# Kernel optimization log

Measured on AMD Instinct MI355X. Metric: run time of the kernel, lower is better.

The kernel has to match this reference:

```python
import jax, jax.numpy as jnp
import numpy as np

B, N, DIM = 1, 1024, 512
H, DH = 8, 64
TOPK_RATIO = 0.1
SCALE = DH ** -0.5
PH = 32  # phase MLP hidden = hidden_dim//2 = 64//2
INIT_SCALE = 0.02


def cayley(Mre, Mim):
    # CayleyLinear: unitary weight W = (I - A)^{-1} (I + A), A skew-Hermitian
    M = (Mre + 1j * Mim).astype(jnp.complex64) * INIT_SCALE
    A = M - M.conj().T
    I = jnp.eye(M.shape[0], dtype=M.dtype)
    return jnp.linalg.solve(I - A, I + A)


def phase_fn(mag, pw1, pb1, pw2, pb2):
    # PhaseModulation: MLP(|alpha|) + 0.1*|alpha| residual
    h = jax.nn.silu(mag[..., None] @ pw1 + pb1)  # (...,PH)
    out = (h @ pw2 + pb2)[..., 0]
    return out + mag * 0.1


def setup_inputs() -> dict:
    key = jax.random.key(0)
    ks = jax.random.split(key, 12)
    d = {
        'x_real': jax.random.normal(ks[0], (B, N, DIM), dtype=jnp.float32),
        'x_imag': jax.random.normal(ks[1], (B, N, DIM), dtype=jnp.float32),
    }
    for i, n in enumerate(['Wq', 'Wk', 'Wv', 'Wo']):
        d[n + '_re'] = jax.random.normal(ks[2 + 2 * i], (DIM, DIM), dtype=jnp.float32)
        d[n + '_im'] = jax.random.normal(ks[3 + 2 * i], (DIM, DIM), dtype=jnp.float32)
    d['pw1'] = jax.random.normal(ks[10], (1, PH), dtype=jnp.float32) * 0.1
    d['pb1'] = jnp.zeros((PH,), dtype=jnp.float32)
    d['pw2'] = jax.random.normal(ks[11], (PH, 1), dtype=jnp.float32) * 0.1
    d['pb2'] = jnp.zeros((1,), dtype=jnp.float32)
    return d


def reference(x_real, x_imag, Wq_re, Wq_im, Wk_re, Wk_im, Wv_re, Wv_im,
              Wo_re, Wo_im, pw1, pb1, pw2, pb2):
    x = (x_real + 1j * x_imag).astype(jnp.complex64)  # (B,N,D)
    Q = x @ cayley(Wq_re, Wq_im)
    K = x @ cayley(Wk_re, Wk_im)
    V = x @ cayley(Wv_re, Wv_im)
    # (B,N,D) -> (B,H,N,DH)
    Q = Q.reshape(B, N, H, DH).transpose(0, 2, 1, 3)
    K = K.reshape(B, N, H, DH).transpose(0, 2, 1, 3)
    V = V.reshape(B, N, H, DH).transpose(0, 2, 1, 3)
    # complex inner products: conj(Q) . K
    alpha = jnp.einsum('bhnd,bhsd->bhns', Q.conj(), K) * SCALE  # (B,H,N,N) complex
    mag = jnp.abs(alpha)
    phase = phase_fn(jax.lax.stop_gradient(mag), pw1, pb1, pw2, pb2)
    beta = alpha * jnp.exp(1j * phase.astype(jnp.complex64))
    # Born-rule normalization: p = |beta|^2 / sum |beta|^2
    b2 = beta.real ** 2 + beta.imag ** 2
    probs = b2 / b2.sum(axis=-1, keepdims=True)  # (B,H,N,N) real
    # top-k interference routing
    k = max(1, int(TOPK_RATIO * N))
    tp, ti = jax.lax.top_k(probs, k)  # (B,H,N,k)
    tpn = tp / (tp.sum(axis=-1, keepdims=True) + 1e-8)
    w = jax.nn.softmax(tpn * k, axis=-1)  # complex_softmax on real input
    # gather V rows per (b,h): (N,DH)[(N,k)] -> (N,k,DH), no NxN expand
    gather = jax.vmap(jax.vmap(lambda v, i: v[i]))
    V_topk = gather(V, ti)  # (B,H,N,k,DH) complex
    out = (w[..., None] * V_topk).sum(axis=3)  # (B,H,N,DH)
    out = out.transpose(0, 2, 1, 3).reshape(B, N, DIM)
    out = out @ cayley(Wo_re, Wo_im)
    return out  # complex64 (B,N,DIM)
```

## Files before the change

### kernel.cpp

```cpp
#include <hip/hip_runtime.h>
#include <math.h>


#define PLANE   262144
#define CMAT    524288
#define PPLANE  524288
#define CPROJ   1048576
#define KTOP    102

#define R_FLOATS 12582912
#define POOL_FLOATS (4*CMAT + 8192 + R_FLOATS)
__device__ __attribute__((aligned(256))) float g_pool[POOL_FLOATS];

__launch_bounds__(256)
__global__ void cgemm_kernel(
    const float* __restrict__ Are, const float* __restrict__ Aim, int sA,
    const float* __restrict__ Bre, const float* __restrict__ Bim, int sB,
    const float* __restrict__ Dre, const float* __restrict__ Dim, int sD,
    const float* __restrict__ Ere2, float* __restrict__ Ewr, int sE,
    float* __restrict__ Cre, float* __restrict__ Cim, int sC,
    int M, int N, int Kd, float dcoef, int mode, int out_floats)
{
    __shared__ float As_re[32][34], As_im[32][34];
    __shared__ float Bs_re[32][68], Bs_im[32][68];
    const int b = blockIdx.z;
    Are += (size_t)b * sA; Aim += (size_t)b * sA;
    Bre += (size_t)b * sB; Bim += (size_t)b * sB;
    Dre += (size_t)b * sD; Dim += (size_t)b * sD;
    const float* Ere = Ere2 + (size_t)b * sE;
    const float* Eim = Ere + PLANE;
    float* Uwr = Ewr ? (Ewr + (size_t)b * sE) : (float*)0;
    Cre += (size_t)b * sC; Cim += (size_t)b * sC;
    const int tid = threadIdx.x;
    const int bm = blockIdx.y * 32, bn = blockIdx.x * 64;
    const int tm = (tid >> 4) << 1;
    const int tn = (tid & 15) << 2;
    const int lmA = tid >> 3;
    const int lkA = (tid & 7) << 2;
    const int lkB = tid >> 4;
    const int lnB = (tid & 15) << 2;
    float cr[2][4] = {{0.f}}, ci[2][4] = {{0.f}};
    const float* pAre = Are + (size_t)(bm + lmA) * Kd + lkA;
    const float* pAim = Aim + (size_t)(bm + lmA) * Kd + lkA;
    const float* pBre = Bre + (size_t)lkB * N + bn + lnB;
    const float* pBim = Bim + (size_t)lkB * N + bn + lnB;
    for (int k0 = 0; k0 < Kd; k0 += 32) {
        const float4 ar = *(const float4*)(pAre + k0);
        const float4 ai = *(const float4*)(pAim + k0);
        const float4 br0 = *(const float4*)(pBre + (size_t)k0 * N);
        const float4 bi0 = *(const float4*)(pBim + (size_t)k0 * N);
        const float4 br1 = *(const float4*)(pBre + (size_t)(k0 + 16) * N);
        const float4 bi1 = *(const float4*)(pBim + (size_t)(k0 + 16) * N);
        __syncthreads();
        As_re[lkA+0][lmA] = ar.x; As_re[lkA+1][lmA] = ar.y;
        As_re[lkA+2][lmA] = ar.z; As_re[lkA+3][lmA] = ar.w;
        As_im[lkA+0][lmA] = ai.x; As_im[lkA+1][lmA] = ai.y;
        As_im[lkA+2][lmA] = ai.z; As_im[lkA+3][lmA] = ai.w;
        *(float4*)&Bs_re[lkB][lnB] = br0;
        *(float4*)&Bs_im[lkB][lnB] = bi0;
        *(float4*)&Bs_re[lkB+16][lnB] = br1;
        *(float4*)&Bs_im[lkB+16][lnB] = bi1;
        __syncthreads();
        #pragma unroll
        for (int k = 0; k < 32; ++k) {
            const float2 xr = *(const float2*)&As_re[k][tm];
            const float2 xi = *(const float2*)&As_im[k][tm];
            const float4 yr = *(const float4*)&Bs_re[k][tn];
            const float4 yi = *(const float4*)&Bs_im[k][tn];
            const float axr[2] = {xr.x, xr.y};
            const float axi[2] = {xi.x, xi.y};
            const float byr[4] = {yr.x, yr.y, yr.z, yr.w};
            const float byi[4] = {yi.x, yi.y, yi.z, yi.w};
            #pragma unroll
            for (int i = 0; i < 2; ++i) {
                #pragma unroll
                for (int j = 0; j < 4; ++j) {
                    cr[i][j] += axr[i]*byr[j] - axi[i]*byi[j];
                    ci[i][j] += axr[i]*byi[j] + axi[i]*byr[j];
                }
            }
        }
    }
    #pragma unroll
    for (int i = 0; i < 2; ++i) {
        const int row = bm + tm + i;
        const size_t idx = (size_t)row * N + bn + tn;
        float vr[4] = {cr[i][0], cr[i][1], cr[i][2], cr[i][3]};
        float vi[4] = {ci[i][0], ci[i][1], ci[i][2], ci[i][3]};
        if (mode == 1) {
            const float4 dr4 = *(const float4*)(Dre + idx);
            const float4 di4 = *(const float4*)(Dim + idx);
            const float dr[4] = {dr4.x, dr4.y, dr4.z, dr4.w};
            const float di[4] = {di4.x, di4.y, di4.z, di4.w};
            #pragma unroll
            for (int j = 0; j < 4; ++j) { vr[j] = dcoef*dr[j] - vr[j]; vi[j] = dcoef*di[j] - vi[j]; }
        } else if (mode == 2) {
            const float4 dr4 = *(const float4*)(Dre + idx);
            const float4 di4 = *(const float4*)(Dim + idx);
            const float dr[4] = {dr4.x, dr4.y, dr4.z, dr4.w};
            const float di[4] = {di4.x, di4.y, di4.z, di4.w};
            float ur[4], ui[4];
            #pragma unroll
            for (int j = 0; j < 4; ++j) { ur[j] = 5.5f*dr[j] + 0.5f*vr[j]; ui[j] = 5.5f*di[j] + 0.5f*vi[j]; }
            *(float4*)(Uwr + idx) = make_float4(ur[0], ur[1], ur[2], ur[3]);
            *(float4*)(Uwr + PLANE + idx) = make_float4(ui[0], ui[1], ui[2], ui[3]);
        } else if (mode == 3) {
            const float inv61 = 1.0f/61.5f;
            const float4 sr4 = *(const float4*)(Dre + idx);
            const float4 si4 = *(const float4*)(Dim + idx);
            const float4 s2r = *(const float4*)(Ere + idx);
            const float4 s2i = *(const float4*)(Eim + idx);
            const float sr[4] = {sr4.x, sr4.y, sr4.z, sr4.w};
            const float si[4] = {si4.x, si4.y, si4.z, si4.w};
            const float tr[4] = {s2r.x, s2r.y, s2r.z, s2r.w};
            const float ti[4] = {s2i.x, s2i.y, s2i.z, s2i.w};
            #pragma unroll
            for (int j = 0; j < 4; ++j) {
                const float diag = (row == bn + tn + j) ? 60.5f : 0.0f;
                vr[j] = (diag + 48.f*sr[j] + 23.f*tr[j] + vr[j]) * inv61;
                vi[j] = (       48.f*si[j] + 23.f*ti[j] + vi[j]) * inv61;
            }
        } else if (mode == 4) {
            const float4 dr4 = *(const float4*)(Dre + idx);
            const float4 di4 = *(const float4*)(Dim + idx);
            const float dr[4] = {dr4.x, dr4.y, dr4.z, dr4.w};
            const float di[4] = {di4.x, di4.y, di4.z, di4.w};
            #pragma unroll
            for (int j = 0; j < 4; ++j) {
                const float diag = (row == bn + tn + j) ? 1.0f : 0.0f;
                vr[j] = 2.f*dr[j] + 2.f*vr[j] - diag;
                vi[j] = 2.f*di[j] + 2.f*vi[j];
            }
        }
        if (mode == 5) {
            #pragma unroll
            for (int j = 0; j < 4; ++j) {
                const size_t ire = idx + j;
                const size_t iim = (size_t)PPLANE + idx + j;
                if (ire < (size_t)out_floats) Cre[ire] = vr[j];
                if (iim < (size_t)out_floats) Cre[iim] = vi[j];
            }
        } else {
            *(float4*)(Cre + idx) = make_float4(vr[0], vr[1], vr[2], vr[3]);
            *(float4*)(Cim + idx) = make_float4(vi[0], vi[1], vi[2], vi[3]);
        }
    }
}

__launch_bounds__(256)
__global__ void build_A_kernel(const float* __restrict__ W0re, const float* __restrict__ W0im,
                               const float* __restrict__ W1re, const float* __restrict__ W1im,
                               const float* __restrict__ W2re, const float* __restrict__ W2im,
                               const float* __restrict__ W3re, const float* __restrict__ W3im,
                               int aoff)
{
    float* Aout = g_pool + aoff;
    const int w = blockIdx.y;
    const float* Mre; const float* Mim;
    if      (w == 0) { Mre = W0re; Mim = W0im; }
    else if (w == 1) { Mre = W1re; Mim = W1im; }
    else if (w == 2) { Mre = W2re; Mim = W2im; }
    else             { Mre = W3re; Mim = W3im; }
    const int idx = blockIdx.x * 256 + threadIdx.x;
    const int i = idx >> 9, j = idx & 511;
    float* Are = Aout + (size_t)w * CMAT;
    float* Aim = Are + PLANE;
    Are[idx] = 0.02f * (Mre[i*512 + j] - Mre[j*512 + i]);
    Aim[idx] = 0.02f * (Mim[i*512 + j] + Mim[j*512 + i]);
}

__launch_bounds__(256)
__global__ void zero_kernel(float* __restrict__ p, int n)
{
    const int i = blockIdx.x * 256 + threadIdx.x;
    if (i < n) p[i] = 0.f;
}

__launch_bounds__(256)
__global__ void scores_kernel(const float* __restrict__ Qre, const float* __restrict__ Qim,
                              const float* __restrict__ Kre, const float* __restrict__ Kim,
                              float* __restrict__ B2, float* __restrict__ RS)
{
    __shared__ float Qs_re[16][68], Qs_im[16][68], Ks_re[16][68], Ks_im[16][68];
    __shared__ float rs[64];
    const int h = blockIdx.z;
    const int bm = blockIdx.y * 64, bn = blockIdx.x * 64;
    const int tid = threadIdx.x;
    const int tm = (tid >> 4) << 2, tn = (tid & 15) << 2;
    const int lm = tid >> 2, lk = (tid & 3) << 2;
    float dr[4][4] = {{0.f}}, di[4][4] = {{0.f}};
    for (int k0 = 0; k0 < 64; k0 += 16) {
        const float4 qr = *(const float4*)(Qre + (size_t)(bm+lm)*512 + h*64 + k0 + lk);
        const float4 qi = *(const float4*)(Qim + (size_t)(bm+lm)*512 + h*64 + k0 + lk);
        const float4 kr = *(const float4*)(Kre + (size_t)(bn+lm)*512 + h*64 + k0 + lk);
        const float4 ki = *(const float4*)(Kim + (size_t)(bn+lm)*512 + h*64 + k0 + lk);
        __syncthreads();
        Qs_re[lk+0][lm]=qr.x; Qs_re[lk+1][lm]=qr.y; Qs_re[lk+2][lm]=qr.z; Qs_re[lk+3][lm]=qr.w;
        Qs_im[lk+0][lm]=qi.x; Qs_im[lk+1][lm]=qi.y; Qs_im[lk+2][lm]=qi.z; Qs_im[lk+3][lm]=qi.w;
        Ks_re[lk+0][lm]=kr.x; Ks_re[lk+1][lm]=kr.y; Ks_re[lk+2][lm]=kr.z; Ks_re[lk+3][lm]=kr.w;
        Ks_im[lk+0][lm]=ki.x; Ks_im[lk+1][lm]=ki.y; Ks_im[lk+2][lm]=ki.z; Ks_im[lk+3][lm]=ki.w;
        __syncthreads();
        #pragma unroll
        for (int k = 0; k < 16; ++k) {
            const float4 xr = *(const float4*)&Qs_re[k][tm];
            const float4 xi = *(const float4*)&Qs_im[k][tm];
            const float4 yr = *(const float4*)&Ks_re[k][tn];
            const float4 yi = *(const float4*)&Ks_im[k][tn];
            const float axr[4] = {xr.x, xr.y, xr.z, xr.w};
            const float axi[4] = {xi.x, xi.y, xi.z, xi.w};
            const float byr[4] = {yr.x, yr.y, yr.z, yr.w};
            const float byi[4] = {yi.x, yi.y, yi.z, yi.w};
            #pragma unroll
            for (int i = 0; i < 4; ++i) {
                #pragma unroll
                for (int j = 0; j < 4; ++j) {
                    dr[i][j] += axr[i]*byr[j] + axi[i]*byi[j];
                    di[i][j] += axr[i]*byi[j] - axi[i]*byr[j];
                }
            }
        }
    }
    if (tid < 64) rs[tid] = 0.f;
    __syncthreads();
    float rpart[4] = {0.f, 0.f, 0.f, 0.f};
    #pragma unroll
    for (int i = 0; i < 4; ++i) {
        #pragma unroll
        for (int j = 0; j < 4; ++j) {
            const float b2v = (dr[i][j]*dr[i][j] + di[i][j]*di[i][j]) * 0.015625f;
            B2[(size_t)h*1048576 + (size_t)(bm+tm+i)*1024 + (bn+tn+j)] = b2v;
            rpart[i] += b2v;
        }
    }
    #pragma unroll
    for (int i = 0; i < 4; ++i) atomicAdd(&rs[tm+i], rpart[i]);
    __syncthreads();
    if (tid < 64) atomicAdd(&RS[h*1024 + bm + tid], rs[tid]);
}

__launch_bounds__(256)
__global__ void select_kernel(const float* __restrict__ B2, const float* __restrict__ RS,
                              const float* __restrict__ Vre, const float* __restrict__ Vim,
                              float* __restrict__ AOre, float* __restrict__ AOim)
{
    __shared__ float sv[1024];
    __shared__ unsigned int hist[256];
    __shared__ int ssum[256];
    __shared__ unsigned int sc[4];
    __shared__ float sel_v[104];
    __shared__ int sel_i[104];
    __shared__ float sel_w[104];
    __shared__ float rbuf[256];
    const int bid = blockIdx.x;
    const int h = bid >> 10, n = bid & 1023;
    const int tid = threadIdx.x;
    const float* row = B2 + (size_t)h * 1048576 + (size_t)n * 1024;
    #pragma unroll
    for (int e = 0; e < 4; ++e) sv[tid + 256*e] = row[tid + 256*e];
    if (tid == 0) sc[2] = 0u;
    __syncthreads();

    unsigned prefix = 0u, pmask = 0u;
    int krem = KTOP;
    for (int pass = 0; pass < 4; ++pass) {
        const int shift = 24 - 8 * pass;
        hist[tid] = 0u;
        __syncthreads();
        #pragma unroll
        for (int e = 0; e < 4; ++e) {
            const unsigned u = __float_as_uint(sv[tid + 256*e]);
            if ((u & pmask) == prefix) atomicAdd(&hist[(u >> shift) & 255u], 1u);
        }
        __syncthreads();
        ssum[tid] = (int)hist[tid];
        __syncthreads();
        for (int off = 1; off < 256; off <<= 1) {
            const int add = (tid + off < 256) ? ssum[tid + off] : 0;
            __syncthreads();
            ssum[tid] += add;
            __syncthreads();
        }
        const int above = (tid < 255) ? ssum[tid + 1] : 0;
        if (ssum[tid] >= krem && above < krem) {
            sc[0] = (unsigned)tid;
            sc[1] = (unsigned)(krem - above);
        }
        __syncthreads();
        prefix |= sc[0] << shift;
        pmask |= 0xFFu << shift;
        krem = (int)sc[1];
        __syncthreads();
    }
    const unsigned T = prefix;
    const int m = krem;

    #pragma unroll
    for (int e = 0; e < 4; ++e) {
        const int i = tid + 256*e;
        const float v = sv[i];
        const unsigned u = __float_as_uint(v);
        bool sel = (u > T);
        if (!sel && u == T) {
            int rank = 0;
            for (int j = 0; j < i; ++j) rank += (__float_as_uint(sv[j]) == T) ? 1 : 0;
            sel = (rank < m);
        }
        if (sel) {
            const unsigned p = atomicAdd(&sc[2], 1u);
            if (p < 104u) { sel_v[p] = v; sel_i[p] = i; }
        }
    }
    __syncthreads();

    rbuf[tid] = (tid < KTOP) ? sel_v[tid] : 0.f;
    __syncthreads();
    for (int st = 128; st > 0; st >>= 1) { if (tid < st) rbuf[tid] += rbuf[tid + st]; __syncthreads(); }
    const float sumtop = rbuf[0];
    __syncthreads();
    rbuf[tid] = (tid < KTOP) ? sel_v[tid] : -1.f;
    __syncthreads();
    for (int st = 128; st > 0; st >>= 1) { if (tid < st) rbuf[tid] = fmaxf(rbuf[tid], rbuf[tid + st]); __syncthreads(); }
    const float vmax = rbuf[0];
    __syncthreads();

    const float S_row = RS[(h << 10) + n];
    const float denom = sumtop + 1e-8f * S_row;
    const float scl = (float)KTOP / denom;
    if (tid < KTOP) sel_w[tid] = expf(sel_v[tid] * scl - vmax * scl);
    __syncthreads();
    rbuf[tid] = (tid < KTOP) ? sel_w[tid] : 0.f;
    __syncthreads();
    for (int st = 128; st > 0; st >>= 1) { if (tid < st) rbuf[tid] += rbuf[tid + st]; __syncthreads(); }
    const float Z = rbuf[0];
    __syncthreads();

    if (tid < 128) {
        const int d = tid & 63;
        const int im = tid >> 6;
        const float* Vp = im ? Vim : Vre;
        const int base = h * 64 + d;
        float acc = 0.f;
        for (int j = 0; j < KTOP; ++j) acc += sel_w[j] * Vp[(size_t)sel_i[j] * 512 + base];
        acc /= Z;
        float* AOp = im ? AOim : AOre;
        AOp[(size_t)n * 512 + h * 64 + d] = acc;
    }
}

extern "C" void kernel_launch(void* const* d_in, const int* in_sizes, int n_in,
                              void* d_out, int out_size, void* d_ws, size_t ws_size,
                              hipStream_t stream)
{
    (void)in_sizes; (void)n_in; (void)d_ws; (void)ws_size;
    const float* x_re = (const float*)d_in[0];
    const float* x_im = (const float*)d_in[1];

    float* pool = nullptr;
    hipGetSymbolAddress((void**)&pool, HIP_SYMBOL(g_pool));

    float* Wall = pool;
    float* RSg  = Wall + 4*CMAT;
    float* R    = RSg + 8192;
    float* A  = R;
    float* S  = R + 4*CMAT;
    float* S2 = R + 8*CMAT;
    float* X  = R + 12*CMAT;
    float* X2 = R + 16*CMAT;
    float* T  = R + 20*CMAT;
    float* Q  = R;
    float* Kp = R + CPROJ;
    float* V  = R + 2*CPROJ;
    float* AO = R + 3*CPROJ;
    float* B2 = R + 4*CPROJ;

    const int aoff = (int)(A - pool);

    build_A_kernel<<<dim3(1024,4),256,0,stream>>>(
        (const float*)d_in[2],(const float*)d_in[3],(const float*)d_in[4],(const float*)d_in[5],
        (const float*)d_in[6],(const float*)d_in[7],(const float*)d_in[8],(const float*)d_in[9], aoff);
    cgemm_kernel<<<dim3(8,16,4),256,0,stream>>>(A,A+PLANE,CMAT, A,A+PLANE,CMAT,
                                                A,A+PLANE,CMAT, A,nullptr,CMAT,
                                                S,S+PLANE,CMAT, 512,512,512, 0.f, 0, 0);
    cgemm_kernel<<<dim3(8,16,4),256,0,stream>>>(S,S+PLANE,CMAT, S,S+PLANE,CMAT,
                                                S,S+PLANE,CMAT, S,X,CMAT,
                                                S2,S2+PLANE,CMAT, 512,512,512, 0.f, 2, 0);
    cgemm_kernel<<<dim3(8,16,4),256,0,stream>>>(S2,S2+PLANE,CMAT, X,X+PLANE,CMAT,
                                                S,S+PLANE,CMAT, S2,nullptr,CMAT,
                                                X2,X2+PLANE,CMAT, 512,512,512, 0.f, 3, 0);
    float* Xc = X2; float* Xn = X;
    for (int it = 0; it < 2; ++it) {
        cgemm_kernel<<<dim3(8,16,4),256,0,stream>>>(S,S+PLANE,CMAT, Xc,Xc+PLANE,CMAT,
                                                    Xc,Xc+PLANE,CMAT, S,nullptr,CMAT,
                                                    T,T+PLANE,CMAT, 512,512,512, 1.f, 1, 0);
        cgemm_kernel<<<dim3(8,16,4),256,0,stream>>>(Xc,Xc+PLANE,CMAT, T,T+PLANE,CMAT,
                                                    Xc,Xc+PLANE,CMAT, S,nullptr,CMAT,
                                                    Xn,Xn+PLANE,CMAT, 512,512,512, 2.f, 1, 0);
        float* tmp = Xc; Xc = Xn; Xn = tmp;
    }
    cgemm_kernel<<<dim3(8,16,4),256,0,stream>>>(A,A+PLANE,CMAT, Xc,Xc+PLANE,CMAT,
                                                Xc,Xc+PLANE,CMAT, S,nullptr,CMAT,
                                                Wall,Wall+PLANE,CMAT, 512,512,512, 0.f, 4, 0);

    cgemm_kernel<<<dim3(8,32,3),256,0,stream>>>(x_re,x_im,0, Wall,Wall+PLANE,CMAT,
                                                x_re,x_im,0, S,nullptr,0,
                                                Q,Q+PPLANE,CPROJ, 1024,512,512, 0.f, 0, 0);

    zero_kernel<<<32,256,0,stream>>>(RSg, 8192);
    scores_kernel<<<dim3(16,16,8),256,0,stream>>>(Q,Q+PPLANE, Kp,Kp+PPLANE, B2, RSg);
    select_kernel<<<8192,256,0,stream>>>(B2, RSg, V,V+PPLANE, AO,AO+PPLANE);

    cgemm_kernel<<<dim3(8,32,1),256,0,stream>>>(AO,AO+PPLANE,0, Wall+3*CMAT,Wall+3*CMAT+PLANE,0,
                                                AO,AO+PPLANE,0, S,nullptr,0,
                                                (float*)d_out,nullptr,0, 1024,512,512, 0.f, 5, out_size);
}
```

Before: 1.027 ms.

## Double-buffer complex GEMM shared tiles and split output GEMM over z

The complex GEMM now keeps two shared-memory buffers and prefetches the next K-tile into registers while computing on the current one, which drops one barrier per iteration and hides global load latency. The final output projection is launched as two batches of 512 rows along z, with per-batch bounds checking on the output size. This doubles shared memory per block, which may reduce occupancy, and makes the mode-5 indexing depend on the batch stride.

```diff
diff --git a/kernel.cpp b/kernel.cpp
--- a/kernel.cpp
+++ b/kernel.cpp
@@ -21,8 +21,8 @@
     float* __restrict__ Cre, float* __restrict__ Cim, int sC,
     int M, int N, int Kd, float dcoef, int mode, int out_floats)
 {
-    __shared__ float As_re[32][34], As_im[32][34];
-    __shared__ float Bs_re[32][68], Bs_im[32][68];
+    __shared__ float As_re[2][32][34], As_im[2][32][34];
+    __shared__ float Bs_re[2][32][68], Bs_im[2][32][68];
     const int b = blockIdx.z;
     Are += (size_t)b * sA; Aim += (size_t)b * sA;
     Bre += (size_t)b * sB; Bim += (size_t)b * sB;
@@ -31,6 +31,7 @@
     const float* Eim = Ere + PLANE;
     float* Uwr = Ewr ? (Ewr + (size_t)b * sE) : (float*)0;
     Cre += (size_t)b * sC; Cim += (size_t)b * sC;
+    const int bnd = mode == 5 ? (out_floats - b * sC) : 0;
     const int tid = threadIdx.x;
     const int bm = blockIdx.y * 32, bn = blockIdx.x * 64;
     const int tm = (tid >> 4) << 1;
@@ -44,29 +45,38 @@
     const float* pAim = Aim + (size_t)(bm + lmA) * Kd + lkA;
     const float* pBre = Bre + (size_t)lkB * N + bn + lnB;
     const float* pBim = Bim + (size_t)lkB * N + bn + lnB;
+    float4 ar  = *(const float4*)(pAre);
+    float4 ai  = *(const float4*)(pAim);
+    float4 br0 = *(const float4*)(pBre);
+    float4 bi0 = *(const float4*)(pBim);
+    float4 br1 = *(const float4*)(pBre + (size_t)16 * N);
+    float4 bi1 = *(const float4*)(pBim + (size_t)16 * N);
     for (int k0 = 0; k0 < Kd; k0 += 32) {
-        const float4 ar = *(const float4*)(pAre + k0);
-        const float4 ai = *(const float4*)(pAim + k0);
-        const float4 br0 = *(const float4*)(pBre + (size_t)k0 * N);
-        const float4 bi0 = *(const float4*)(pBim + (size_t)k0 * N);
-        const float4 br1 = *(const float4*)(pBre + (size_t)(k0 + 16) * N);
-        const float4 bi1 = *(const float4*)(pBim + (size_t)(k0 + 16) * N);
-        __syncthreads();
-        As_re[lkA+0][lmA] = ar.x; As_re[lkA+1][lmA] = ar.y;
-        As_re[lkA+2][lmA] = ar.z; As_re[lkA+3][lmA] = ar.w;
-        As_im[lkA+0][lmA] = ai.x; As_im[lkA+1][lmA] = ai.y;
-        As_im[lkA+2][lmA] = ai.z; As_im[lkA+3][lmA] = ai.w;
-        *(float4*)&Bs_re[lkB][lnB] = br0;
-        *(float4*)&Bs_im[lkB][lnB] = bi0;
-        *(float4*)&Bs_re[lkB+16][lnB] = br1;
-        *(float4*)&Bs_im[lkB+16][lnB] = bi1;
-        __syncthreads();
+        const int buf = (k0 >> 5) & 1;
+        As_re[buf][lkA+0][lmA] = ar.x; As_re[buf][lkA+1][lmA] = ar.y;
+        As_re[buf][lkA+2][lmA] = ar.z; As_re[buf][lkA+3][lmA] = ar.w;
+        As_im[buf][lkA+0][lmA] = ai.x; As_im[buf][lkA+1][lmA] = ai.y;
+        As_im[buf][lkA+2][lmA] = ai.z; As_im[buf][lkA+3][lmA] = ai.w;
+        *(float4*)&Bs_re[buf][lkB][lnB] = br0;
+        *(float4*)&Bs_im[buf][lkB][lnB] = bi0;
+        *(float4*)&Bs_re[buf][lkB+16][lnB] = br1;
+        *(float4*)&Bs_im[buf][lkB+16][lnB] = bi1;
+        __syncthreads();
+        const int kn = k0 + 32;
+        if (kn < Kd) {
+            ar  = *(const float4*)(pAre + kn);
+            ai  = *(const float4*)(pAim + kn);
+            br0 = *(const float4*)(pBre + (size_t)kn * N);
+            bi0 = *(const float4*)(pBim + (size_t)kn * N);
+            br1 = *(const float4*)(pBre + (size_t)(kn + 16) * N);
+            bi1 = *(const float4*)(pBim + (size_t)(kn + 16) * N);
+        }
         #pragma unroll
         for (int k = 0; k < 32; ++k) {
-            const float2 xr = *(const float2*)&As_re[k][tm];
-            const float2 xi = *(const float2*)&As_im[k][tm];
-            const float4 yr = *(const float4*)&Bs_re[k][tn];
-            const float4 yi = *(const float4*)&Bs_im[k][tn];
+            const float2 xr = *(const float2*)&As_re[buf][k][tm];
+            const float2 xi = *(const float2*)&As_im[buf][k][tm];
+            const float4 yr = *(const float4*)&Bs_re[buf][k][tn];
+            const float4 yi = *(const float4*)&Bs_im[buf][k][tn];
             const float axr[2] = {xr.x, xr.y};
             const float axi[2] = {xi.x, xi.y};
             const float byr[4] = {yr.x, yr.y, yr.z, yr.w};
@@ -137,8 +147,8 @@
             for (int j = 0; j < 4; ++j) {
                 const size_t ire = idx + j;
                 const size_t iim = (size_t)PPLANE + idx + j;
-                if (ire < (size_t)out_floats) Cre[ire] = vr[j];
-                if (iim < (size_t)out_floats) Cre[iim] = vi[j];
+                if (ire < (size_t)bnd) Cre[ire] = vr[j];
+                if (iim < (size_t)bnd) Cre[iim] = vi[j];
             }
         } else {
             *(float4*)(Cre + idx) = make_float4(vr[0], vr[1], vr[2], vr[3]);
@@ -409,7 +419,7 @@
     scores_kernel<<<dim3(16,16,8),256,0,stream>>>(Q,Q+PPLANE, Kp,Kp+PPLANE, B2, RSg);
     select_kernel<<<8192,256,0,stream>>>(B2, RSg, V,V+PPLANE, AO,AO+PPLANE);
 
-    cgemm_kernel<<<dim3(8,32,1),256,0,stream>>>(AO,AO+PPLANE,0, Wall+3*CMAT,Wall+3*CMAT+PLANE,0,
+    cgemm_kernel<<<dim3(8,16,2),256,0,stream>>>(AO,AO+PPLANE,PLANE, Wall+3*CMAT,Wall+3*CMAT+PLANE,0,
                                                 AO,AO+PPLANE,0, S,nullptr,0,
-                                                (float*)d_out,nullptr,0, 1024,512,512, 0.f, 5, out_size);
-}
+                                                (float*)d_out,nullptr,PLANE, 512,512,512, 0.f, 5, out_size);
+}
```

After: 1.003 ms. 1.02x faster.
